# Kernel tuning notes

Measured on AMD Instinct MI355X. Metric: run time of the kernel, lower is better.

## Reference

```python
import jax, jax.numpy as jnp
import numpy as np

N, OBS, ENC, ACT, K = 16384, 512, 512, 64, 8
ALPHA = 1.0


def setup_inputs() -> dict:
    key = jax.random.key(0)
    ks = jax.random.split(key, 8)
    s = 0.05  # keep activations/logits well-scaled
    return {
        "X1": jax.random.normal(ks[0], (N, OBS), jnp.float32),
        "X0": jax.random.normal(ks[1], (N, OBS), jnp.float32),
        "U": jax.random.normal(ks[2], (N, ACT), jnp.float32),
        "W_enc": jax.random.normal(ks[3], (ENC, OBS), jnp.float32) * s,
        "A_all": jax.random.normal(ks[4], (K, ENC, ENC), jnp.float32) * s,
        "B_rest": jax.random.normal(ks[5], (K - 1, ACT, ENC), jnp.float32) * s,
        "C_w": jax.random.normal(ks[6], (K, ENC), jnp.float32) * s,
        "C_b": jax.random.normal(ks[7], (K,), jnp.float32) * s,
    }


def reference(X1, X0, U, W_enc, A_all, B_rest, C_w, C_b):
    enc_dim = W_enc.shape[0]
    act_dim = U.shape[1]
    k = A_all.shape[0]
    # encoder: bias-free linear
    X1e = X1 @ W_enc.T  # [N, enc]
    X0e = X0 @ W_enc.T  # [N, enc]
    # gating: argmax of linear classifier C
    inds = jnp.argmax(X0e @ C_w.T + C_b, axis=1)  # [N]
    # expert 0 uses fixed B0 = eye(enc)[:act, :]; experts 1..k-1 learned
    B0 = jnp.eye(enc_dim, dtype=X0.dtype)[:act_dim]  # [act, enc]
    B_all = jnp.concatenate([B0[None], B_rest], axis=0)  # [k, act, enc]
    # per-expert predictions for every row (nn.Linear: x @ W.T -> einsum over input dim h)
    preds = jnp.einsum('nh,keh->kne', X0e, A_all) + jnp.einsum('na,kae->kne', U, B_all)
    # squared error per (expert, row), then select each row's routed expert
    sq = jnp.sum((X1e[None, :, :] - preds) ** 2, axis=-1)  # [k, N]
    onehot = jax.nn.one_hot(inds, k, dtype=sq.dtype)  # [N, k]
    loss = ALPHA * jnp.sum(sq * onehot.T)
    return loss / (enc_dim * X1.shape[0])
```

## Files before the change

### kernel.cpp

```cpp
#include <hip/hip_runtime.h>

#define NROWS 16384
#define OBSD 512
#define ENCD 512
#define ACTD 64
#define KEXP 8

typedef __attribute__((ext_vector_type(8))) short bf16x8;
typedef __attribute__((ext_vector_type(4))) float f32x4;
typedef __attribute__((address_space(3))) unsigned char lds_byte;
typedef __attribute__((address_space(1))) unsigned char glb_byte;

__device__ __forceinline__ unsigned short f2bf(float f) {
  unsigned int u = __float_as_uint(f);
  u = (u + 0x7FFFu + ((u >> 16) & 1u)) >> 16;
  return (unsigned short)u;
}
__device__ __forceinline__ unsigned int cvtpk(float lo, float hi) {
  unsigned int r;
  asm("v_cvt_pk_bf16_f32 %0, %1, %2" : "=v"(r) : "v"(lo), "v"(hi));
  return r;
}
__device__ __forceinline__ void gload_lds16(const unsigned short* g, unsigned short* l) {
  __builtin_amdgcn_global_load_lds((const glb_byte*)g, (lds_byte*)l, 16, 0, 0);
}

__global__ __launch_bounds__(256) void gt_k(
    const float* __restrict__ W, const float* __restrict__ Cw,
    float* __restrict__ GT, float* __restrict__ loss,
    int* __restrict__ counts, int* __restrict__ cursor) {
  const int b = blockIdx.x, tid = threadIdx.x;
  if (b == 0) {
    if (tid == 0) *loss = 0.f;
    if (tid < KEXP) { counts[tid] = 0; cursor[tid] = 0; }
  }
  __shared__ float red[4][64];
  int e = b >> 3, o0 = (b & 7) * 64;
  int o = tid & 63, hg = tid >> 6;
  float s = 0.f;
#pragma unroll 8
  for (int h = hg * 128; h < hg * 128 + 128; h++)
    s += Cw[e * ENCD + h] * W[(size_t)h * OBSD + o0 + o];
  red[hg][o] = s;
  __syncthreads();
  if (tid < 64)
    GT[(o0 + tid) * KEXP + e] = red[0][tid] + red[1][tid] + red[2][tid] + red[3][tid];
}

__global__ __launch_bounds__(256) void fused_prep_k(
    const float* __restrict__ X0, const float* __restrict__ X1,
    const float* __restrict__ U, const float* __restrict__ W,
    const float* __restrict__ Brest, const float* __restrict__ GT,
    const float* __restrict__ Cb,
    unsigned short* __restrict__ X0bf, unsigned short* __restrict__ X1bf,
    unsigned short* __restrict__ Ubf, unsigned short* __restrict__ Wbf,
    unsigned short* __restrict__ BfTN, unsigned short* __restrict__ WbfT,
    int* __restrict__ inds, int* __restrict__ counts) {
  const int b = blockIdx.x, tid = threadIdx.x;
  if (b < 512) {
    __shared__ int lhist[KEXP];
    if (tid < KEXP) lhist[tid] = 0;
    __syncthreads();
    const int lane = tid & 63, w = tid >> 6;
    float g[8][8];
    const float* gp = GT + lane * 8 * KEXP;
#pragma unroll
    for (int j = 0; j < 8; j++) {
      float4 lo = *(const float4*)(gp + j * KEXP);
      float4 hi = *(const float4*)(gp + j * KEXP + 4);
      g[j][0] = lo.x; g[j][1] = lo.y; g[j][2] = lo.z; g[j][3] = lo.w;
      g[j][4] = hi.x; g[j][5] = hi.y; g[j][6] = hi.z; g[j][7] = hi.w;
    }
    float cb[KEXP];
#pragma unroll
    for (int e = 0; e < KEXP; e++) cb[e] = Cb[e];
#pragma unroll 2
    for (int r = 0; r < 8; r++) {
      const int n = b * 32 + w * 8 + r;
      const float4* xr = (const float4*)(X0 + (size_t)n * OBSD + lane * 8);
      float4 x = xr[0], y = xr[1];
      float xv[8] = {x.x, x.y, x.z, x.w, y.x, y.y, y.z, y.w};
      float acc[KEXP] = {};
#pragma unroll
      for (int j = 0; j < 8; j++)
#pragma unroll
        for (int e = 0; e < KEXP; e++) acc[e] += xv[j] * g[j][e];
      uint4 rr = {cvtpk(x.x, x.y), cvtpk(x.z, x.w), cvtpk(y.x, y.y), cvtpk(y.z, y.w)};
      *(uint4*)&X0bf[(size_t)n * OBSD + lane * 8] = rr;
#pragma unroll
      for (int e = 0; e < KEXP; e++) {
#pragma unroll
        for (int off = 32; off > 0; off >>= 1) acc[e] += __shfl_xor(acc[e], off, 64);
      }
      if (lane == 0) {
        int best = 0;
        float bv = acc[0] + cb[0];
#pragma unroll
        for (int e = 1; e < KEXP; e++) {
          float v = acc[e] + cb[e];
          if (v > bv) { bv = v; best = e; }
        }
        inds[n] = best;
        atomicAdd(&lhist[best], 1);
      }
    }
    __syncthreads();
    if (tid < KEXP) atomicAdd(&counts[tid], lhist[tid]);
    return;
  }
  if (b < 4608) {
    size_t i = ((size_t)(b - 512) * 256 + tid) * 8;
    const float4* s4 = (const float4*)(X1 + i);
    float4 a = s4[0], c = s4[1];
    uint4 r = {cvtpk(a.x, a.y), cvtpk(a.z, a.w), cvtpk(c.x, c.y), cvtpk(c.z, c.w)};
    *(uint4*)&X1bf[i] = r;
    return;
  }
  if (b < 4664) {
    __shared__ float tile[64][65];
    int t = b - 4608;
    int k = (t >> 3);
    int e0 = (t & 7) * 64;
    const float* src = Brest + (size_t)k * ACTD * ENCD + e0;
#pragma unroll
    for (int j = 0; j < 16; j++) {
      int idx = j * 256 + tid;
      int a = idx >> 6, e = idx & 63;
      tile[a][e] = src[(size_t)a * ENCD + e];
    }
    __syncthreads();
    unsigned short* dst = BfTN + ((size_t)(k + 1) * ENCD + e0) * ACTD;
#pragma unroll
    for (int j = 0; j < 16; j++) {
      int idx = j * 256 + tid;
      int e = idx >> 6, a = idx & 63;
      dst[(size_t)e * ACTD + a] = f2bf(-tile[a][e]);
    }
    return;
  }
  if (b == 4664) {
    for (int j = 0; j < 16; j++) {
      int i8 = j * 256 + tid;
      int e = i8 >> 3, a0 = (i8 & 7) * 8;
      unsigned int w0 = 0, w1 = 0, w2 = 0, w3 = 0;
      if (e >= a0 && e < a0 + 8) {
        unsigned int bits = 0xBF80u << ((e & 1) * 16);
        if ((e - a0) >> 1 == 0) w0 = bits;
        else if ((e - a0) >> 1 == 1) w1 = bits;
        else if ((e - a0) >> 1 == 2) w2 = bits;
        else w3 = bits;
      }
      uint4 v = {w0, w1, w2, w3};
      *(uint4*)&BfTN[(size_t)i8 * 8] = v;
    }
    return;
  }
  if (b < 5945) {
    int cb2 = b - 4665;
    if (cb2 < 1024) {
      size_t i = (size_t)cb2 * 256 + tid;
      float4 v = ((const float4*)U)[i];
      uint2 r = {cvtpk(v.x, v.y), cvtpk(v.z, v.w)};
      *(uint2*)&Ubf[i * 4] = r;
    } else {
      size_t i = (size_t)(cb2 - 1024) * 256 + tid;
      float4 v = ((const float4*)W)[i];
      uint2 r = {cvtpk(v.x, v.y), cvtpk(v.z, v.w)};
      *(uint2*)&Wbf[i * 4] = r;
    }
    return;
  }
  {
    __shared__ float tile[64][65];
    int t = b - 5945;
    int h0 = (t >> 3) * 64, o0 = (t & 7) * 64;
#pragma unroll
    for (int j = 0; j < 16; j++) {
      int idx = j * 256 + tid;
      int a = idx >> 6, e = idx & 63;
      tile[a][e] = W[(size_t)(h0 + a) * OBSD + o0 + e];
    }
    __syncthreads();
#pragma unroll
    for (int j = 0; j < 16; j++) {
      int idx = j * 256 + tid;
      int e = idx >> 6, a = idx & 63;
      WbfT[(size_t)(o0 + e) * OBSD + h0 + a] = f2bf(tile[a][e]);
    }
  }
}

__global__ __launch_bounds__(256, 2) void scatmgemm_k(
    const int* __restrict__ inds, const int* __restrict__ counts,
    int* __restrict__ cursor, int* __restrict__ rowlist,
    const float* __restrict__ Aall, const unsigned short* __restrict__ WbfT,
    unsigned short* __restrict__ MN) {
  if (blockIdx.x < 64) {
    __shared__ int lhist[KEXP], lbase[KEXP], sstart[KEXP];
    const int tid = threadIdx.x;
    if (tid < KEXP) {
      lhist[tid] = 0;
      int s = 0;
      for (int j = 0; j < KEXP; j++) {
        if (j == tid) sstart[tid] = s;
        s += counts[j];
      }
    }
    __syncthreads();
    const int n = blockIdx.x * 256 + tid;
    const int r = inds[n];
    const int lpos = atomicAdd(&lhist[r], 1);
    __syncthreads();
    if (tid < KEXP) lbase[tid] = atomicAdd(&cursor[tid], lhist[tid]);
    __syncthreads();
    rowlist[sstart[r] + lbase[r] + lpos] = n;
    return;
  }
  __shared__ unsigned short As[128 * 32];
  __shared__ unsigned short Bs[128 * 32];
  const int tid = threadIdx.x;
  const int t = blockIdx.x - 64;
  const int k = t >> 4;
  const int rem = t & 15;
  const int row0 = (rem >> 2) * 128;
  const int col0 = (rem & 3) * 128;

  const int lane = tid & 63, w = tid >> 6;
  const int wr = w >> 1, wc = w & 1;
  const int srow = tid >> 1, sj = tid & 1;
  const int swz = (srow >> 1) & 3;
  const int wo0 = srow * 32 + ((2 * sj) ^ swz) * 8;
  const int wo1 = srow * 32 + ((2 * sj + 1) ^ swz) * 8;
  const int gslot = ((tid & 3) ^ ((tid >> 3) & 3)) * 8;
  const int srowB = tid >> 2;
  const int ldsoff = tid * 8;
  const int rslot = ((lane >> 4) ^ (((lane & 15) >> 1) & 3)) * 8;
  const int arow = wr * 64 + (lane & 15);
  const int brow = wc * 64 + (lane & 15);
  const float* pA = Aall + ((size_t)k * ENCD + row0 + srow) * ENCD + sj * 16;

  f32x4 acc[4][4] = {};
  for (int k0 = 0; k0 < ENCD; k0 += 32) {
    float4 a0 = *(const float4*)(pA + k0);
    float4 a1 = *(const float4*)(pA + k0 + 4);
    float4 a2 = *(const float4*)(pA + k0 + 8);
    float4 a3 = *(const float4*)(pA + k0 + 12);
    uint4 pa0 = {cvtpk(-a0.x, -a0.y), cvtpk(-a0.z, -a0.w),
                 cvtpk(-a1.x, -a1.y), cvtpk(-a1.z, -a1.w)};
    uint4 pa1 = {cvtpk(-a2.x, -a2.y), cvtpk(-a2.z, -a2.w),
                 cvtpk(-a3.x, -a3.y), cvtpk(-a3.z, -a3.w)};
    *(uint4*)&As[wo0] = pa0;
    *(uint4*)&As[wo1] = pa1;
    gload_lds16(WbfT + (size_t)(col0 + srowB) * OBSD + k0 + gslot, &Bs[ldsoff]);
    gload_lds16(WbfT + (size_t)(col0 + 64 + srowB) * OBSD + k0 + gslot, &Bs[2048 + ldsoff]);
    __syncthreads();
    bf16x8 af[4], bfr[4];
#pragma unroll
    for (int m = 0; m < 4; m++) af[m] = *(const bf16x8*)&As[(arow + m * 16) * 32 + rslot];
#pragma unroll
    for (int n = 0; n < 4; n++) bfr[n] = *(const bf16x8*)&Bs[(brow + n * 16) * 32 + rslot];
#pragma unroll
    for (int m = 0; m < 4; m++)
#pragma unroll
      for (int n = 0; n < 4; n++)
        acc[m][n] = __builtin_amdgcn_mfma_f32_16x16x32_bf16(bfr[n], af[m], acc[m][n], 0, 0, 0);
    __syncthreads();
  }
  unsigned short* Mk = MN + (size_t)k * ENCD * OBSD;
#pragma unroll
  for (int m = 0; m < 4; m++) {
    int rowg = row0 + wr * 64 + m * 16 + (lane & 15);
#pragma unroll
    for (int n = 0; n < 4; n++) {
      int colg = col0 + wc * 64 + n * 16 + (lane >> 4) * 4;
      uint2 v = {cvtpk(acc[m][n][0], acc[m][n][1]), cvtpk(acc[m][n][2], acc[m][n][3])};
      *(uint2*)&Mk[(size_t)rowg * OBSD + colg] = v;
    }
  }
}

__global__ __launch_bounds__(256, 2) void grouped_mfma_k(
    const unsigned short* __restrict__ X1bf, const unsigned short* __restrict__ X0bf,
    const unsigned short* __restrict__ Wbf, const unsigned short* __restrict__ Ubf,
    const unsigned short* __restrict__ MN, const unsigned short* __restrict__ BfTN,
    const int* __restrict__ rowlist, const int* __restrict__ counts,
    float* __restrict__ loss) {
  const int tid = threadIdx.x;
  const int bid = blockIdx.x;
  const int lid = (bid & 7) * 512 + (bid >> 3);
  const int k = lid >> 9;
  const int rem = lid & 511;
  const int col0 = (rem & 3) * 128;
  const int tile = rem >> 2;

  int start = 0, cnt = 0;
#pragma unroll
  for (int j = 0; j < KEXP; j++) {
    int c = counts[j];
    if (j < k) start += c;
    if (j == k) cnt = c;
  }
  if (tile * 128 >= cnt) return;

  __shared__ unsigned short As[128 * 64];
  __shared__ unsigned short Bs[128 * 64];
  __shared__ int ridx[128];
  __shared__ float red[4];

  if (tid < 128) {
    int p = tile * 128 + tid;
    ridx[tid] = rowlist[start + (p < cnt ? p : 0)];
  }
  __syncthreads();

  const int lane = tid & 63, w = tid >> 6;
  const int wr = w >> 1, wc = w & 1;
  const int srow8 = tid >> 3;
  const int lslot = ((tid & 7) ^ (srow8 & 7)) * 8;
  const int ldsoff = tid * 8;
  const int r15 = lane & 15;
  const int qk = lane >> 4;
  const int rsw = r15 & 7;
  const int arow = wr * 64 + r15;
  const int brow = wc * 64 + r15;
  int rnj[4];
#pragma unroll
  for (int j = 0; j < 4; j++) rnj[j] = ridx[j * 32 + srow8];

  const unsigned short* MkN = MN + (size_t)k * ENCD * OBSD;
  const unsigned short* BfTkN = BfTN + (size_t)k * ENCD * ACTD;

  f32x4 acc[4][4] = {};
#define GROUPED_COMPUTE()                                                            \
  do {                                                                               \
    __syncthreads();                                                                 \
    _Pragma("unroll") for (int kk = 0; kk < 2; kk++) {                               \
      const int ps = ((kk * 4 + qk) ^ rsw) * 8;                                      \
      bf16x8 af[4], bfr[4];                                                          \
      _Pragma("unroll") for (int m = 0; m < 4; m++)                                  \
          af[m] = *(const bf16x8*)&As[(arow + m * 16) * 64 + ps];                    \
      _Pragma("unroll") for (int n = 0; n < 4; n++)                                  \
          bfr[n] = *(const bf16x8*)&Bs[(brow + n * 16) * 64 + ps];                   \
      _Pragma("unroll") for (int m = 0; m < 4; m++)                                  \
          _Pragma("unroll") for (int n = 0; n < 4; n++)                              \
              acc[m][n] = __builtin_amdgcn_mfma_f32_16x16x32_bf16(bfr[n], af[m],     \
                                                                  acc[m][n], 0, 0, 0); \
    }                                                                                \
    __syncthreads();                                                                 \
  } while (0)

  for (int k0 = 0; k0 < OBSD; k0 += 64) {
#pragma unroll
    for (int j = 0; j < 4; j++) {
      int row = j * 32 + srow8;
      gload_lds16(X1bf + (size_t)rnj[j] * OBSD + k0 + lslot, &As[j * 2048 + ldsoff]);
      gload_lds16(Wbf + (size_t)(col0 + row) * OBSD + k0 + lslot, &Bs[j * 2048 + ldsoff]);
    }
    GROUPED_COMPUTE();
  }
  for (int k0 = 0; k0 < OBSD; k0 += 64) {
#pragma unroll
    for (int j = 0; j < 4; j++) {
      int row = j * 32 + srow8;
      gload_lds16(X0bf + (size_t)rnj[j] * OBSD + k0 + lslot, &As[j * 2048 + ldsoff]);
      gload_lds16(MkN + (size_t)(col0 + row) * OBSD + k0 + lslot, &Bs[j * 2048 + ldsoff]);
    }
    GROUPED_COMPUTE();
  }
  {
#pragma unroll
    for (int j = 0; j < 4; j++) {
      int row = j * 32 + srow8;
      gload_lds16(Ubf + (size_t)rnj[j] * ACTD + lslot, &As[j * 2048 + ldsoff]);
      gload_lds16(BfTkN + (size_t)(col0 + row) * ACTD + lslot, &Bs[j * 2048 + ldsoff]);
    }
    GROUPED_COMPUTE();
  }
#undef GROUPED_COMPUTE

  float sq = 0.f;
#pragma unroll
  for (int m = 0; m < 4; m++) {
    int lr = wr * 64 + m * 16 + r15;
    if (tile * 128 + lr < cnt) {
#pragma unroll
      for (int n = 0; n < 4; n++)
        sq += acc[m][n][0] * acc[m][n][0] + acc[m][n][1] * acc[m][n][1] +
              acc[m][n][2] * acc[m][n][2] + acc[m][n][3] * acc[m][n][3];
    }
  }
#pragma unroll
  for (int off = 32; off > 0; off >>= 1) sq += __shfl_xor(sq, off, 64);
  if (lane == 0) red[w] = sq;
  __syncthreads();
  if (tid == 0) atomicAdd(loss, red[0] + red[1] + red[2] + red[3]);
}

__global__ void finalize_k(const float* __restrict__ loss, float* __restrict__ out) {
  if (threadIdx.x == 0 && blockIdx.x == 0)
    out[0] = loss[0] * (1.0f / ((float)ENCD * (float)NROWS));
}

extern "C" void kernel_launch(void* const* d_in, const int* in_sizes, int n_in,
                              void* d_out, int out_size, void* d_ws, size_t ws_size,
                              hipStream_t stream) {
  const float* X1 = (const float*)d_in[0];
  const float* X0 = (const float*)d_in[1];
  const float* U = (const float*)d_in[2];
  const float* W = (const float*)d_in[3];
  const float* Aall = (const float*)d_in[4];
  const float* Brest = (const float*)d_in[5];
  const float* Cw = (const float*)d_in[6];
  const float* Cb = (const float*)d_in[7];
  float* out = (float*)d_out;

  char* p = (char*)d_ws;
  auto alloc = [&](size_t bytes) { char* r = p; p += (bytes + 255) & ~(size_t)255; return r; };
  unsigned short* X1bf = (unsigned short*)alloc((size_t)NROWS * OBSD * 2);
  unsigned short* X0bf = (unsigned short*)alloc((size_t)NROWS * OBSD * 2);
  unsigned short* Ubf = (unsigned short*)alloc((size_t)NROWS * ACTD * 2);
  unsigned short* Wbf = (unsigned short*)alloc((size_t)ENCD * OBSD * 2);
  unsigned short* BfTN = (unsigned short*)alloc((size_t)KEXP * ENCD * ACTD * 2);
  unsigned short* WbfT = (unsigned short*)alloc((size_t)OBSD * ENCD * 2);
  unsigned short* MN = (unsigned short*)alloc((size_t)KEXP * ENCD * OBSD * 2);
  float* GT = (float*)alloc(KEXP * OBSD * 4);
  float* loss = (float*)alloc(256);
  int* inds = (int*)alloc(NROWS * 4);
  int* rowlist = (int*)alloc(NROWS * 4);
  int* counts = (int*)alloc(64);
  int* cursor = (int*)alloc(64);

  gt_k<<<64, 256, 0, stream>>>(W, Cw, GT, loss, counts, cursor);
  fused_prep_k<<<6009, 256, 0, stream>>>(X0, X1, U, W, Brest, GT, Cb,
                                         X0bf, X1bf, Ubf, Wbf, BfTN, WbfT,
                                         inds, counts);
  scatmgemm_k<<<192, 256, 0, stream>>>(inds, counts, cursor, rowlist,
                                       Aall, WbfT, MN);
  grouped_mfma_k<<<4096, 256, 0, stream>>>(X1bf, X0bf, Wbf, Ubf, MN, BfTN,
                                           rowlist, counts, loss);
  finalize_k<<<1, 64, 0, stream>>>(loss, out);
}
```

Baseline: 84.99 us.

## Move W transpose into gt_k and fold M=A·W GEMM into prep kernel

```diff
diff --git a/kernel.cpp b/kernel.cpp
--- a/kernel.cpp
+++ b/kernel.cpp
@@ -27,34 +27,54 @@
 
 __global__ __launch_bounds__(256) void gt_k(
     const float* __restrict__ W, const float* __restrict__ Cw,
-    float* __restrict__ GT, float* __restrict__ loss,
-    int* __restrict__ counts, int* __restrict__ cursor) {
+    float* __restrict__ GT, unsigned short* __restrict__ WbfT,
+    float* __restrict__ loss, int* __restrict__ counts, int* __restrict__ cursor) {
   const int b = blockIdx.x, tid = threadIdx.x;
-  if (b == 0) {
-    if (tid == 0) *loss = 0.f;
-    if (tid < KEXP) { counts[tid] = 0; cursor[tid] = 0; }
-  }
-  __shared__ float red[4][64];
-  int e = b >> 3, o0 = (b & 7) * 64;
-  int o = tid & 63, hg = tid >> 6;
-  float s = 0.f;
+  if (b < 64) {
+    if (b == 0) {
+      if (tid == 0) *loss = 0.f;
+      if (tid < KEXP) { counts[tid] = 0; cursor[tid] = 0; }
+    }
+    __shared__ float red[4][64];
+    int e = b >> 3, o0 = (b & 7) * 64;
+    int o = tid & 63, hg = tid >> 6;
+    float s = 0.f;
 #pragma unroll 8
-  for (int h = hg * 128; h < hg * 128 + 128; h++)
-    s += Cw[e * ENCD + h] * W[(size_t)h * OBSD + o0 + o];
-  red[hg][o] = s;
-  __syncthreads();
-  if (tid < 64)
-    GT[(o0 + tid) * KEXP + e] = red[0][tid] + red[1][tid] + red[2][tid] + red[3][tid];
+    for (int h = hg * 128; h < hg * 128 + 128; h++)
+      s += Cw[e * ENCD + h] * W[(size_t)h * OBSD + o0 + o];
+    red[hg][o] = s;
+    __syncthreads();
+    if (tid < 64)
+      GT[(o0 + tid) * KEXP + e] = red[0][tid] + red[1][tid] + red[2][tid] + red[3][tid];
+    return;
+  }
+  __shared__ float tile[64][65];
+  int t = b - 64;
+  int h0 = (t >> 3) * 64, o0 = (t & 7) * 64;
+#pragma unroll
+  for (int j = 0; j < 16; j++) {
+    int idx = j * 256 + tid;
+    int a = idx >> 6, e = idx & 63;
+    tile[a][e] = W[(size_t)(h0 + a) * OBSD + o0 + e];
+  }
+  __syncthreads();
+#pragma unroll
+  for (int j = 0; j < 16; j++) {
+    int idx = j * 256 + tid;
+    int e = idx >> 6, a = idx & 63;
+    WbfT[(size_t)(o0 + e) * OBSD + h0 + a] = f2bf(tile[a][e]);
+  }
 }
 
 __global__ __launch_bounds__(256) void fused_prep_k(
     const float* __restrict__ X0, const float* __restrict__ X1,
     const float* __restrict__ U, const float* __restrict__ W,
-    const float* __restrict__ Brest, const float* __restrict__ GT,
-    const float* __restrict__ Cb,
+    const float* __restrict__ Aall, const float* __restrict__ Brest,
+    const float* __restrict__ GT, const float* __restrict__ Cb,
+    const unsigned short* __restrict__ WbfT,
     unsigned short* __restrict__ X0bf, unsigned short* __restrict__ X1bf,
     unsigned short* __restrict__ Ubf, unsigned short* __restrict__ Wbf,
-    unsigned short* __restrict__ BfTN, unsigned short* __restrict__ WbfT,
+    unsigned short* __restrict__ BfTN, unsigned short* __restrict__ MN,
     int* __restrict__ inds, int* __restrict__ counts) {
   const int b = blockIdx.x, tid = threadIdx.x;
   if (b < 512) {
@@ -117,7 +137,7 @@
     return;
   }
   if (b < 4664) {
-    __shared__ float tile[64][65];
+    __shared__ float tileB[64][65];
     int t = b - 4608;
     int k = (t >> 3);
     int e0 = (t & 7) * 64;
@@ -126,7 +146,7 @@
     for (int j = 0; j < 16; j++) {
       int idx = j * 256 + tid;
       int a = idx >> 6, e = idx & 63;
-      tile[a][e] = src[(size_t)a * ENCD + e];
+      tileB[a][e] = src[(size_t)a * ENCD + e];
     }
     __syncthreads();
     unsigned short* dst = BfTN + ((size_t)(k + 1) * ENCD + e0) * ACTD;
@@ -134,7 +154,7 @@
     for (int j = 0; j < 16; j++) {
       int idx = j * 256 + tid;
       int e = idx >> 6, a = idx & 63;
-      dst[(size_t)e * ACTD + a] = f2bf(-tile[a][e]);
+      dst[(size_t)e * ACTD + a] = f2bf(-tileB[a][e]);
     }
     return;
   }
@@ -170,56 +190,9 @@
     }
     return;
   }
-  {
-    __shared__ float tile[64][65];
-    int t = b - 5945;
-    int h0 = (t >> 3) * 64, o0 = (t & 7) * 64;
-#pragma unroll
-    for (int j = 0; j < 16; j++) {
-      int idx = j * 256 + tid;
-      int a = idx >> 6, e = idx & 63;
-      tile[a][e] = W[(size_t)(h0 + a) * OBSD + o0 + e];
-    }
-    __syncthreads();
-#pragma unroll
-    for (int j = 0; j < 16; j++) {
-      int idx = j * 256 + tid;
-      int e = idx >> 6, a = idx & 63;
-      WbfT[(size_t)(o0 + e) * OBSD + h0 + a] = f2bf(tile[a][e]);
-    }
-  }
-}
-
-__global__ __launch_bounds__(256, 2) void scatmgemm_k(
-    const int* __restrict__ inds, const int* __restrict__ counts,
-    int* __restrict__ cursor, int* __restrict__ rowlist,
-    const float* __restrict__ Aall, const unsigned short* __restrict__ WbfT,
-    unsigned short* __restrict__ MN) {
-  if (blockIdx.x < 64) {
-    __shared__ int lhist[KEXP], lbase[KEXP], sstart[KEXP];
-    const int tid = threadIdx.x;
-    if (tid < KEXP) {
-      lhist[tid] = 0;
-      int s = 0;
-      for (int j = 0; j < KEXP; j++) {
-        if (j == tid) sstart[tid] = s;
-        s += counts[j];
-      }
-    }
-    __syncthreads();
-    const int n = blockIdx.x * 256 + tid;
-    const int r = inds[n];
-    const int lpos = atomicAdd(&lhist[r], 1);
-    __syncthreads();
-    if (tid < KEXP) lbase[tid] = atomicAdd(&cursor[tid], lhist[tid]);
-    __syncthreads();
-    rowlist[sstart[r] + lbase[r] + lpos] = n;
-    return;
-  }
   __shared__ unsigned short As[128 * 32];
   __shared__ unsigned short Bs[128 * 32];
-  const int tid = threadIdx.x;
-  const int t = blockIdx.x - 64;
+  const int t = b - 5945;
   const int k = t >> 4;
   const int rem = t & 15;
   const int row0 = (rem >> 2) * 128;
@@ -277,6 +250,29 @@
       *(uint2*)&Mk[(size_t)rowg * OBSD + colg] = v;
     }
   }
+}
+
+__global__ __launch_bounds__(256) void scatter_k(
+    const int* __restrict__ inds, const int* __restrict__ counts,
+    int* __restrict__ cursor, int* __restrict__ rowlist) {
+  __shared__ int lhist[KEXP], lbase[KEXP], sstart[KEXP];
+  const int tid = threadIdx.x;
+  if (tid < KEXP) {
+    lhist[tid] = 0;
+    int s = 0;
+    for (int j = 0; j < KEXP; j++) {
+      if (j == tid) sstart[tid] = s;
+      s += counts[j];
+    }
+  }
+  __syncthreads();
+  const int n = blockIdx.x * 256 + tid;
+  const int r = inds[n];
+  const int lpos = atomicAdd(&lhist[r], 1);
+  __syncthreads();
+  if (tid < KEXP) lbase[tid] = atomicAdd(&cursor[tid], lhist[tid]);
+  __syncthreads();
+  rowlist[sstart[r] + lbase[r] + lpos] = n;
 }
 
 __global__ __launch_bounds__(256, 2) void grouped_mfma_k(
@@ -430,12 +426,11 @@
   int* counts = (int*)alloc(64);
   int* cursor = (int*)alloc(64);
 
-  gt_k<<<64, 256, 0, stream>>>(W, Cw, GT, loss, counts, cursor);
-  fused_prep_k<<<6009, 256, 0, stream>>>(X0, X1, U, W, Brest, GT, Cb,
-                                         X0bf, X1bf, Ubf, Wbf, BfTN, WbfT,
+  gt_k<<<128, 256, 0, stream>>>(W, Cw, GT, WbfT, loss, counts, cursor);
+  fused_prep_k<<<6073, 256, 0, stream>>>(X0, X1, U, W, Aall, Brest, GT, Cb,
+                                         WbfT, X0bf, X1bf, Ubf, Wbf, BfTN, MN,
                                          inds, counts);
-  scatmgemm_k<<<192, 256, 0, stream>>>(inds, counts, cursor, rowlist,
-                                       Aall, WbfT, MN);
+  scatter_k<<<64, 256, 0, stream>>>(inds, counts, cursor, rowlist);
   grouped_mfma_k<<<4096, 256, 0, stream>>>(X1bf, X0bf, Wbf, Ubf, MN, BfTN,
                                            rowlist, counts, loss);
   finalize_k<<<1, 64, 0, stream>>>(loss, out);
```

New measurement: 89.97 us. 1.06x slower.
